# Kernel optimization log

Hardware: AMD Instinct MI355X
Metric: run time of the kernel (lower is better)

Reference implementation:

```python
import jax, jax.numpy as jnp
import numpy as np

N = 50000          # nodes
E = 1_600_000      # edges
IN = 256           # in_channels
C = 32             # hidden_channels (per-head width)
HEADS = 4
BN_EPS = 1e-5


def setup_inputs() -> dict:
    key = jax.random.key(0)
    ks = jax.random.split(key, 32)
    g = lambda k, shp, s=0.1: (jax.random.normal(k, shp, jnp.float32) * s)
    inp = {
        "x": jax.random.normal(ks[0], (N, IN), jnp.float32),
        "edge_index": jax.random.randint(ks[1], (2, E), 0, N, jnp.int64),
        "edge_attr": jax.random.uniform(ks[2], (E, 1), jnp.float32),
        # conv1 (GATConv in=IN, out=C, heads=HEADS, edge_dim=1)
        "W1": g(ks[3], (IN, HEADS * C)),
        "as1": g(ks[4], (HEADS, C)),
        "ad1": g(ks[5], (HEADS, C)),
        "We1": g(ks[6], (1, HEADS * C)),
        "ae1": g(ks[7], (HEADS, C)),
        "b1": jnp.zeros((HEADS * C,), jnp.float32),
        # bn1 (eval mode, running_mean=0, running_var=1)
        "g1": jnp.ones((HEADS * C,), jnp.float32),
        "be1": jnp.zeros((HEADS * C,), jnp.float32),
        # conv2 (GATConv in=HEADS*C, out=C, heads=1, concat=False, edge_dim=1)
        "W2": g(ks[8], (HEADS * C, C)),
        "as2": g(ks[9], (1, C)),
        "ad2": g(ks[10], (1, C)),
        "We2": g(ks[11], (1, C)),
        "ae2": g(ks[12], (1, C)),
        "b2": jnp.zeros((C,), jnp.float32),
        # bn2
        "g2": jnp.ones((C,), jnp.float32),
        "be2": jnp.zeros((C,), jnp.float32),
        # classifier: Linear(C,16) -> ReLU -> Linear(16,2)
        "Wc1": g(ks[13], (C, 16)),
        "bc1": jnp.zeros((16,), jnp.float32),
        "Wc2": g(ks[14], (16, 2)),
        "bc2": jnp.zeros((2,), jnp.float32),
        "Wr1": g(ks[15], (C, 16)),
        "br1": jnp.zeros((16,), jnp.float32),
        "Wr2": g(ks[16], (16, 1)),
        "br2": jnp.zeros((1,), jnp.float32),
    }
    return inp


def _gat_conv(x, src, dst, eattr, W, a_src, a_dst, We, a_e, bias, heads, c, concat):
    n = x.shape[0]
    xs = (x @ W).reshape(n, heads, c)                       # [N,H,C]
    al_s = (xs * a_src).sum(-1)                              # [N,H]
    al_d = (xs * a_dst).sum(-1)                              # [N,H]
    ee = (eattr @ We).reshape(-1, heads, c)                  # [E,H,C]
    al_e = (ee * a_e).sum(-1)                                # [E,H]
    alpha = al_s[src] + al_d[dst] + al_e                     # [E,H]
    alpha = jax.nn.leaky_relu(alpha, 0.2)
    # segment softmax over destination node
    mx = jax.ops.segment_max(alpha, dst, num_segments=n)
    ex = jnp.exp(alpha - mx[dst])
    den = jax.ops.segment_sum(ex, dst, num_segments=n)
    a = ex / (den[dst] + 1e-16)                              # [E,H]
    out = jax.ops.segment_sum(xs[src] * a[..., None], dst, num_segments=n)  # [N,H,C]
    out = out.reshape(n, heads * c) if concat else out.mean(axis=1)
    return out + bias


def _add_self_loops(src, dst, eattr, n):
    loop = jnp.arange(n, dtype=src.dtype)
    fill = jnp.broadcast_to(eattr.mean(axis=0, keepdims=True), (n, eattr.shape[1]))
    return (jnp.concatenate([src, loop]), jnp.concatenate([dst, loop]),
            jnp.concatenate([eattr, fill], axis=0))


def _bn_eval(x, gamma, beta):
    # running_mean=0, running_var=1 (fresh BatchNorm1d, eval mode)
    return x * (gamma / jnp.sqrt(1.0 + BN_EPS)) + beta


def reference(x, edge_index, edge_attr, W1, as1, ad1, We1, ae1, b1, g1, be1,
              W2, as2, ad2, We2, ae2, b2, g2, be2,
              Wc1, bc1, Wc2, bc2, Wr1, br1, Wr2, br2):
    n = x.shape[0]
    src, dst, ea = _add_self_loops(edge_index[0], edge_index[1], edge_attr, n)
    h = _gat_conv(x, src, dst, ea, W1, as1, ad1, We1, ae1, b1, HEADS, C, True)
    h = jax.nn.elu(_bn_eval(h, g1, be1))
    h = _gat_conv(h, src, dst, ea, W2, as2, ad2, We2, ae2, b2, 1, C, False)
    h = jax.nn.elu(_bn_eval(h, g2, be2))
    cls = jax.nn.relu(h @ Wc1 + bc1) @ Wc2 + bc2             # [N,2]
    reg = (jax.nn.relu(h @ Wr1 + br1) @ Wr2 + br2)[:, 0]     # [N]
    return cls, reg, h
```

## Files before the change

### kernel.cpp

```cpp
#include <hip/hip_runtime.h>
#include <cstdint>
#include <cstddef>

#define NN 50000
#define EE 1600000
#define IN_DIM 256
#define HC 128
#define CD 32
#define BN_RS 0.9999950000374997f

#define CAP1 96
#define CAP2 128
#define NBKT 196
#define S1_B 782
#define HIST_B 320
#define G1_B 782

typedef __attribute__((ext_vector_type(8))) short short8;
typedef __attribute__((ext_vector_type(4))) float f32x4;

__device__ __forceinline__ float lrelu(float a) { return a > 0.f ? a : 0.2f * a; }
__device__ __forceinline__ float elu(float a) { return a > 0.f ? a : (__expf(a) - 1.f); }

__device__ __forceinline__ unsigned short f2bf(float f) {
    unsigned int u = __float_as_uint(f);
    unsigned int r = (u + 0x7FFFu + ((u >> 16) & 1u)) >> 16;
    return (unsigned short)r;
}
__device__ __forceinline__ float bf2f(unsigned short b) {
    return __uint_as_float(((unsigned int)b) << 16);
}
__device__ __forceinline__ float2 bf2f2(unsigned int p) {
    float2 r;
    r.x = __uint_as_float(p << 16);
    r.y = __uint_as_float(p & 0xFFFF0000u);
    return r;
}
__device__ __forceinline__ void unpack_edge(unsigned long long p, int& s, float& eav) {
    s = (int)(unsigned int)(p & 0xFFFFFFFFull);
    eav = __uint_as_float((unsigned int)(p >> 32));
}
__device__ __forceinline__ float pick4(float a, float b, float c, float d, int h) {
    return (h & 2) ? ((h & 1) ? d : c) : ((h & 1) ? b : a);
}

__device__ __forceinline__ int block_excl_scan_256(int v, int tid, int* wsum) {
    int lane = tid & 63, wv = tid >> 6;
    int x = v;
    #pragma unroll
    for (int off = 1; off < 64; off <<= 1) {
        int y = __shfl_up(x, off);
        if (lane >= off) x += y;
    }
    if (lane == 63) wsum[wv] = x;
    __syncthreads();
    int wpre = 0;
    #pragma unroll
    for (int w = 0; w < 4; w++)
        if (w < wv) wpre += wsum[w];
    return wpre + x - v;
}

__global__ __launch_bounds__(256) void k0_prep(const float* __restrict__ W1,
                                               const float* __restrict__ W2,
                                               const float* __restrict__ We1,
                                               const float* __restrict__ ae1,
                                               const float* __restrict__ We2,
                                               const float* __restrict__ ae2,
                                               unsigned short* __restrict__ W1hi,
                                               unsigned short* __restrict__ W1lo,
                                               unsigned short* __restrict__ W2hi,
                                               unsigned short* __restrict__ W2lo,
                                               float* __restrict__ consts,
                                               int* __restrict__ bucketHist,
                                               int* __restrict__ bucketCursor,
                                               int* __restrict__ indptr) {
    int blk = blockIdx.x;
    int tid = threadIdx.x;
    if (blk < 16) {
        int t = blk * 256 + tid;
        int lane = t & 63;
        int kt = (t >> 6) & 7;
        int nt = t >> 9;
        int kbase = kt * 32 + (lane >> 4) * 8;
        int col = nt * 16 + (lane & 15);
        size_t obase = (size_t)t * 8;
        #pragma unroll
        for (int j = 0; j < 8; j++) {
            float w = W1[(size_t)(kbase + j) * HC + col];
            unsigned short h = f2bf(w);
            W1hi[obase + j] = h;
            W1lo[obase + j] = f2bf(w - bf2f(h));
        }
    } else if (blk < 18) {
        int t = (blk - 16) * 256 + tid;
        int lane = t & 63;
        int kt = (t >> 6) & 3;
        int nt = t >> 8;
        int kbase = kt * 32 + (lane >> 4) * 8;
        int col = nt * 16 + (lane & 15);
        size_t obase = (size_t)t * 8;
        #pragma unroll
        for (int j = 0; j < 8; j++) {
            float w = W2[(size_t)(kbase + j) * CD + col];
            unsigned short h = f2bf(w);
            W2hi[obase + j] = h;
            W2lo[obase + j] = f2bf(w - bf2f(h));
        }
    } else {
        if (tid < NBKT) { bucketHist[tid] = 0; bucketCursor[tid] = 0; }
        if (tid == 200) consts[0] = 0.f;
        if (tid == 201) indptr[NN] = EE;
        if (tid < 4) {
            float s = 0.f;
            for (int c = 0; c < 32; c++) s += We1[tid * 32 + c] * ae1[tid * 32 + c];
            consts[2 + tid] = s;
        } else if (tid == 4) {
            float s = 0.f;
            for (int c = 0; c < 32; c++) s += We2[c] * ae2[c];
            consts[6] = s;
        }
    }
}

__global__ __launch_bounds__(256) void kA_hist_gemm1(const int* __restrict__ ei,
                                                     const float* __restrict__ ea,
                                                     const float* __restrict__ x,
                                                     const unsigned short* __restrict__ Whi,
                                                     const unsigned short* __restrict__ Wlo,
                                                     int* __restrict__ bucketHist,
                                                     float* __restrict__ easum,
                                                     unsigned short* __restrict__ xs1b) {
    __shared__ int h[256];
    int tid = threadIdx.x;
    if (blockIdx.x < HIST_B) {
        h[tid] = 0;
        __syncthreads();
        float s = 0.f;
        for (int i = blockIdx.x * 256 + tid; i < EE; i += HIST_B * 256) {
            atomicAdd(&h[ei[EE + i] >> 8], 1);
            s += ea[i];
        }
        __syncthreads();
        if (tid < NBKT && h[tid] > 0) atomicAdd(&bucketHist[tid], h[tid]);
        #pragma unroll
        for (int off = 32; off > 0; off >>= 1) s += __shfl_xor(s, off);
        if ((tid & 63) == 0) atomicAdd(easum, s);
    } else {
        int lane = tid & 63, wv = tid >> 6;
        int row0 = (blockIdx.x - HIST_B) * 64 + wv * 16;
        if (row0 >= NN) return;
        int m = lane & 15;
        int q = lane >> 4;
        f32x4 acc[8];
        #pragma unroll
        for (int nt = 0; nt < 8; nt++) acc[nt] = {0.f, 0.f, 0.f, 0.f};
        const float* xrow = x + (size_t)(row0 + m) * IN_DIM + q * 8;
        #pragma unroll
        for (int kt = 0; kt < 8; kt++) {
            float4 v0 = *(const float4*)(xrow + kt * 32);
            float4 v1 = *(const float4*)(xrow + kt * 32 + 4);
            float vv[8] = {v0.x, v0.y, v0.z, v0.w, v1.x, v1.y, v1.z, v1.w};
            short8 ahi, alo;
            #pragma unroll
            for (int j = 0; j < 8; j++) {
                unsigned short hh = f2bf(vv[j]);
                ahi[j] = (short)hh;
                alo[j] = (short)f2bf(vv[j] - bf2f(hh));
            }
            #pragma unroll
            for (int nt = 0; nt < 8; nt++) {
                size_t fb = ((size_t)(nt * 8 + kt) * 64 + lane) * 8;
                short8 bhi = *(const short8*)(Whi + fb);
                short8 blo = *(const short8*)(Wlo + fb);
                acc[nt] = __builtin_amdgcn_mfma_f32_16x16x32_bf16(ahi, bhi, acc[nt], 0, 0, 0);
                acc[nt] = __builtin_amdgcn_mfma_f32_16x16x32_bf16(ahi, blo, acc[nt], 0, 0, 0);
                acc[nt] = __builtin_amdgcn_mfma_f32_16x16x32_bf16(alo, bhi, acc[nt], 0, 0, 0);
            }
        }
        #pragma unroll
        for (int nt = 0; nt < 8; nt++) {
            #pragma unroll
            for (int rg = 0; rg < 4; rg++) {
                int row = row0 + q * 4 + rg;
                xs1b[(size_t)row * HC + nt * 16 + m] = f2bf(acc[nt][rg]);
            }
        }
    }
}

__global__ __launch_bounds__(256) void kB_stage1_al1(const int* __restrict__ ei,
                                                     const float* __restrict__ ea,
                                                     const int* __restrict__ bucketHist,
                                                     int* __restrict__ bucketCursor,
                                                     uint2* __restrict__ Apack,
                                                     const unsigned short* __restrict__ xs1b,
                                                     const float* __restrict__ as1,
                                                     const float* __restrict__ ad1,
                                                     float* __restrict__ als,
                                                     float* __restrict__ ald) {
    __shared__ int cnt[256];
    __shared__ int basel[256];
    __shared__ int gbase[256];
    __shared__ int wsum[4];
    __shared__ int wsum2[4];
    __shared__ int sdst[2048];
    __shared__ int ssrc[2048];
    __shared__ float sea[2048];
    int tid = threadIdx.x;
    if (blockIdx.x < S1_B) {
        cnt[tid] = 0;
        int hv = (tid < NBKT) ? bucketHist[tid] : 0;
        int hexcl = block_excl_scan_256(hv, tid, wsum2);
        int base = blockIdx.x * 2048;
        int d[8], s[8], r[8], bk[8];
        float e[8];
        #pragma unroll
        for (int k = 0; k < 8; k++) {
            int i = base + k * 256 + tid;
            if (i < EE) {
                d[k] = ei[EE + i];
                s[k] = ei[i];
                e[k] = ea[i];
                bk[k] = d[k] >> 8;
                r[k] = atomicAdd(&cnt[bk[k]], 1);
            } else d[k] = -1;
        }
        __syncthreads();
        int v = cnt[tid];
        int excl = block_excl_scan_256(v, tid, wsum);
        basel[tid] = excl;
        if (tid < NBKT) gbase[tid] = hexcl + atomicAdd(&bucketCursor[tid], v);
        __syncthreads();
        #pragma unroll
        for (int k = 0; k < 8; k++) {
            if (d[k] >= 0) {
                int slot = basel[bk[k]] + r[k];
                sdst[slot] = d[k];
                ssrc[slot] = s[k];
                sea[slot] = e[k];
            }
        }
        __syncthreads();
        int total = basel[255] + cnt[255];
        for (int slot = tid; slot < total; slot += 256) {
            int dd = sdst[slot];
            int b = dd >> 8;
            int pos = gbase[b] + (slot - basel[b]);
            Apack[pos] = make_uint2((unsigned int)ssrc[slot] | ((unsigned int)(dd & 255) << 24),
                                    __float_as_uint(sea[slot]));
        }
    } else {
        int t = (blockIdx.x - S1_B) * 256 + tid;
        if (t < NN * 4) {
            int hh = t & 3;
            const unsigned int* xp = (const unsigned int*)(xs1b + (size_t)t * 32);
            const float* ap = as1 + hh * 32;
            const float* dp = ad1 + hh * 32;
            float s = 0.f, d = 0.f;
            #pragma unroll
            for (int q = 0; q < 16; q++) {
                float2 v = bf2f2(xp[q]);
                s += v.x * ap[q * 2] + v.y * ap[q * 2 + 1];
                d += v.x * dp[q * 2] + v.y * dp[q * 2 + 1];
            }
            als[t] = s;
            ald[t] = d;
        }
    }
}

__global__ __launch_bounds__(1024) void stage2_kernel(const int* __restrict__ bucketHist,
                                                      const uint2* __restrict__ Apack,
                                                      int* __restrict__ indptr,
                                                      unsigned long long* __restrict__ edgedat,
                                                      float* __restrict__ consts) {
    __shared__ int cnt[256];
    __shared__ int dbase[256];
    __shared__ int s_start;
    int tid = threadIdx.x;
    int b = blockIdx.x;
    if (b == 0 && tid == 0) consts[1] = consts[0] / (float)EE;
    if (tid < 64) {
        int p = 0;
        for (int i = tid; i < b; i += 64) p += bucketHist[i];
        #pragma unroll
        for (int off = 32; off > 0; off >>= 1) p += __shfl_xor(p, off);
        if (tid == 0) s_start = p;
    }
    if (tid < 256) cnt[tid] = 0;
    __syncthreads();
    int start = s_start;
    int end = start + bucketHist[b];
    for (int i = start + tid; i < end; i += 1024) atomicAdd(&cnt[Apack[i].x >> 24], 1);
    __syncthreads();
    if (tid < 64) {
        int b4 = tid * 4;
        int c0 = cnt[b4], c1 = cnt[b4 + 1], c2 = cnt[b4 + 2], c3 = cnt[b4 + 3];
        int t = c0 + c1 + c2 + c3;
        int x = t;
        #pragma unroll
        for (int off = 1; off < 64; off <<= 1) {
            int y = __shfl_up(x, off);
            if (tid >= off) x += y;
        }
        int e0 = x - t;
        dbase[b4] = e0;
        dbase[b4 + 1] = e0 + c0;
        dbase[b4 + 2] = e0 + c0 + c1;
        dbase[b4 + 3] = e0 + c0 + c1 + c2;
    }
    __syncthreads();
    if (tid < 256) {
        int n = b * 256 + tid;
        if (n < NN) indptr[n] = start + dbase[tid];
        cnt[tid] = 0;
    }
    __syncthreads();
    for (int i = start + tid; i < end; i += 1024) {
        uint2 p = Apack[i];
        int dl = p.x >> 24;
        int r = atomicAdd(&cnt[dl], 1);
        int pos = start + dbase[dl] + r;
        edgedat[pos] = (unsigned long long)(p.x & 0xFFFFFFu) |
                       ((unsigned long long)p.y << 32);
    }
}

#define ACC4(vv, ww) { float2 p0_ = bf2f2((vv).x); float2 p1_ = bf2f2((vv).y); \
    acc0 += p0_.x * (ww); acc1 += p0_.y * (ww); acc2 += p1_.x * (ww); acc3 += p1_.y * (ww); }

#define H1P 136
__global__ __launch_bounds__(256, 8) void gat1_gemm2(
    const unsigned short* __restrict__ xs1b, const float* __restrict__ als,
    const float* __restrict__ ald, const unsigned long long* __restrict__ edgedat,
    const int* __restrict__ indptr, const float* __restrict__ consts,
    const float* __restrict__ b1, const float* __restrict__ g1,
    const float* __restrict__ be1,
    const unsigned short* __restrict__ W2hi, const unsigned short* __restrict__ W2lo,
    const float* __restrict__ as2, const float* __restrict__ ad2,
    unsigned short* __restrict__ xs2b, float* __restrict__ als2,
    float* __restrict__ ald2) {
    __shared__ __align__(16) float exbuf[8][CAP1][4];
    __shared__ int srcbuf[8][CAP1];
    __shared__ __align__(16) unsigned short h1hi_s[8][H1P];
    __shared__ __align__(16) unsigned short h1lo_s[8][H1P];
    int tid = threadIdx.x;
    int l = tid & 31;
    int nb = tid >> 5;
    int n = blockIdx.x * 8 + nb;
    int start = indptr[n];
    int deg = indptr[n + 1] - start;
    float ea_mean = consts[1];
    float ce0 = consts[2], ce1 = consts[3], ce2 = consts[4], ce3 = consts[5];
    float4 a4d = *(const float4*)(ald + (size_t)n * 4);
    float4 a4s = *(const float4*)(als + (size_t)n * 4);
    float ex00 = __expf(lrelu(a4s.x + a4d.x + ea_mean * ce0));
    float ex01 = __expf(lrelu(a4s.y + a4d.y + ea_mean * ce1));
    float ex02 = __expf(lrelu(a4s.z + a4d.z + ea_mean * ce2));
    float ex03 = __expf(lrelu(a4s.w + a4d.w + ea_mean * ce3));
    float sm0 = 0.f, sm1 = 0.f, sm2 = 0.f, sm3 = 0.f;
    const unsigned long long* edp = edgedat + start;
    for (int i = l; i < deg; i += 32) {
        int s; float eav;
        unpack_edge(edp[i], s, eav);
        float4 v4 = *(const float4*)(als + (size_t)s * 4);
        float4 ex4;
        ex4.x = __expf(lrelu(v4.x + a4d.x + eav * ce0)); sm0 += ex4.x;
        ex4.y = __expf(lrelu(v4.y + a4d.y + eav * ce1)); sm1 += ex4.y;
        ex4.z = __expf(lrelu(v4.z + a4d.z + eav * ce2)); sm2 += ex4.z;
        ex4.w = __expf(lrelu(v4.w + a4d.w + eav * ce3)); sm3 += ex4.w;
        if (i < CAP1) {
            srcbuf[nb][i] = s * (HC * 2);
            *(float4*)(&exbuf[nb][i][0]) = ex4;
        }
    }
    #pragma unroll
    for (int off = 16; off > 0; off >>= 1) {
        sm0 += __shfl_xor(sm0, off);
        sm1 += __shfl_xor(sm1, off);
        sm2 += __shfl_xor(sm2, off);
        sm3 += __shfl_xor(sm3, off);
    }
    int h2 = l >> 3;
    float ex0sel = pick4(ex00, ex01, ex02, ex03, h2);
    float inv = 1.0f / (pick4(sm0, sm1, sm2, sm3, h2) + ex0sel + 1e-16f);
    int mcap = deg < CAP1 ? deg : CAP1;
    const char* xb = (const char*)xs1b + (size_t)l * 8;
    float acc0, acc1, acc2, acc3;
    {
        uint2 v = *(const uint2*)(xb + (size_t)n * (HC * 2));
        float2 p0 = bf2f2(v.x), p1 = bf2f2(v.y);
        acc0 = p0.x * ex0sel; acc1 = p0.y * ex0sel;
        acc2 = p1.x * ex0sel; acc3 = p1.y * ex0sel;
    }
    int i = 0;
    for (; i + 8 <= mcap; i += 8) {
        int o0 = srcbuf[nb][i + 0], o1 = srcbuf[nb][i + 1];
        int o2 = srcbuf[nb][i + 2], o3 = srcbuf[nb][i + 3];
        int o4 = srcbuf[nb][i + 4], o5 = srcbuf[nb][i + 5];
        int o6 = srcbuf[nb][i + 6], o7 = srcbuf[nb][i + 7];
        float w0 = exbuf[nb][i + 0][h2], w1 = exbuf[nb][i + 1][h2];
        float w2 = exbuf[nb][i + 2][h2], w3 = exbuf[nb][i + 3][h2];
        float w4 = exbuf[nb][i + 4][h2], w5 = exbuf[nb][i + 5][h2];
        float w6 = exbuf[nb][i + 6][h2], w7 = exbuf[nb][i + 7][h2];
        uint2 v0 = *(const uint2*)(xb + o0);
        uint2 v1 = *(const uint2*)(xb + o1);
        uint2 v2 = *(const uint2*)(xb + o2);
        uint2 v3 = *(const uint2*)(xb + o3);
        uint2 v4 = *(const uint2*)(xb + o4);
        uint2 v5 = *(const uint2*)(xb + o5);
        uint2 v6 = *(const uint2*)(xb + o6);
        uint2 v7 = *(const uint2*)(xb + o7);
        ACC4(v0, w0); ACC4(v1, w1); ACC4(v2, w2); ACC4(v3, w3);
        ACC4(v4, w4); ACC4(v5, w5); ACC4(v6, w6); ACC4(v7, w7);
    }
    for (; i < mcap; i++) {
        int o = srcbuf[nb][i];
        float w = exbuf[nb][i][h2];
        uint2 v = *(const uint2*)(xb + o);
        ACC4(v, w);
    }
    if (deg > CAP1) {
        float aldsel = pick4(a4d.x, a4d.y, a4d.z, a4d.w, h2);
        float cesel = pick4(ce0, ce1, ce2, ce3, h2);
        for (int j = CAP1; j < deg; j++) {
            int s; float eav;
            unpack_edge(edp[j], s, eav);
            float w = __expf(lrelu(als[(size_t)s * 4 + h2] + aldsel + eav * cesel));
            uint2 v = *(const uint2*)(xb + (size_t)s * (HC * 2));
            ACC4(v, w);
        }
    }
    acc0 *= inv; acc1 *= inv; acc2 *= inv; acc3 *= inv;
    int c = l * 4;
    float4 bb = *(const float4*)(b1 + c);
    float4 gg = *(const float4*)(g1 + c);
    float4 eb = *(const float4*)(be1 + c);
    float o0 = elu((acc0 + bb.x) * (gg.x * BN_RS) + eb.x);
    float o1 = elu((acc1 + bb.y) * (gg.y * BN_RS) + eb.y);
    float o2 = elu((acc2 + bb.z) * (gg.z * BN_RS) + eb.z);
    float o3 = elu((acc3 + bb.w) * (gg.w * BN_RS) + eb.w);
    unsigned short h0 = f2bf(o0), h1v = f2bf(o1), h2v = f2bf(o2), h3v = f2bf(o3);
    unsigned short l0 = f2bf(o0 - bf2f(h0)), l1 = f2bf(o1 - bf2f(h1v));
    unsigned short l2 = f2bf(o2 - bf2f(h2v)), l3 = f2bf(o3 - bf2f(h3v));
    uint2 hiw, low;
    hiw.x = (unsigned int)h0 | ((unsigned int)h1v << 16);
    hiw.y = (unsigned int)h2v | ((unsigned int)h3v << 16);
    low.x = (unsigned int)l0 | ((unsigned int)l1 << 16);
    low.y = (unsigned int)l2 | ((unsigned int)l3 << 16);
    *(uint2*)(&h1hi_s[nb][c]) = hiw;
    *(uint2*)(&h1lo_s[nb][c]) = low;
    __syncthreads();
    if (tid >= 64) return;

    int lane = tid;
    int m = lane & 15, q = lane >> 4;
    int r8 = m & 7;
    f32x4 g2acc0 = {0.f, 0.f, 0.f, 0.f};
    f32x4 g2acc1 = {0.f, 0.f, 0.f, 0.f};
    #pragma unroll
    for (int kt = 0; kt < 4; kt++) {
        short8 ahi = *(const short8*)(&h1hi_s[r8][q * 8 + kt * 32]);
        short8 alo = *(const short8*)(&h1lo_s[r8][q * 8 + kt * 32]);
        size_t fb0 = ((size_t)kt * 64 + lane) * 8;
        size_t fb1 = ((size_t)(4 + kt) * 64 + lane) * 8;
        short8 bhi0 = *(const short8*)(W2hi + fb0);
        short8 blo0 = *(const short8*)(W2lo + fb0);
        short8 bhi1 = *(const short8*)(W2hi + fb1);
        short8 blo1 = *(const short8*)(W2lo + fb1);
        g2acc0 = __builtin_amdgcn_mfma_f32_16x16x32_bf16(ahi, bhi0, g2acc0, 0, 0, 0);
        g2acc0 = __builtin_amdgcn_mfma_f32_16x16x32_bf16(ahi, blo0, g2acc0, 0, 0, 0);
        g2acc0 = __builtin_amdgcn_mfma_f32_16x16x32_bf16(alo, bhi0, g2acc0, 0, 0, 0);
        g2acc1 = __builtin_amdgcn_mfma_f32_16x16x32_bf16(ahi, bhi1, g2acc1, 0, 0, 0);
        g2acc1 = __builtin_amdgcn_mfma_f32_16x16x32_bf16(ahi, blo1, g2acc1, 0, 0, 0);
        g2acc1 = __builtin_amdgcn_mfma_f32_16x16x32_bf16(alo, bhi1, g2acc1, 0, 0, 0);
    }
    int n0 = blockIdx.x * 8;
    float a0 = as2[m], a1 = as2[m + 16];
    float d0 = ad2[m], d1 = ad2[m + 16];
    #pragma unroll
    for (int rg = 0; rg < 4; rg++) {
        int rloc = q * 4 + rg;
        float s = g2acc0[rg] * a0 + g2acc1[rg] * a1;
        float d = g2acc0[rg] * d0 + g2acc1[rg] * d1;
        #pragma unroll
        for (int off = 1; off < 16; off <<= 1) {
            s += __shfl_xor(s, off);
            d += __shfl_xor(d, off);
        }
        if (rloc < 8) {
            int row = n0 + rloc;
            xs2b[(size_t)row * CD + m]      = f2bf(g2acc0[rg]);
            xs2b[(size_t)row * CD + 16 + m] = f2bf(g2acc1[rg]);
            if (m == 0) { als2[row] = s; ald2[row] = d; }
        }
    }
}

__global__ __launch_bounds__(256) void gat2_agg(
    const unsigned short* __restrict__ xs2b, const float* __restrict__ als,
    const float* __restrict__ ald, const unsigned long long* __restrict__ edgedat,
    const int* __restrict__ indptr, const float* __restrict__ consts,
    const float* __restrict__ b2, const float* __restrict__ g2, const float* __restrict__ be2,
    const float* __restrict__ Wc1, const float* __restrict__ bc1,
    const float* __restrict__ Wc2, const float* __restrict__ bc2,
    const float* __restrict__ Wr1, const float* __restrict__ br1,
    const float* __restrict__ Wr2, const float* __restrict__ br2,
    float* __restrict__ hout, float* __restrict__ cls, float* __restrict__ reg) {
    __shared__ float exbuf[4][CAP2];
    __shared__ int srcbuf[4][CAP2];
    __shared__ __align__(16) float hbuf[4][32];
    int wv = threadIdx.x >> 6;
    int lane = threadIdx.x & 63;
    int n = blockIdx.x * 4 + wv;
    int start = indptr[n];
    int deg = indptr[n + 1] - start;
    float ea_mean = consts[1];
    float ce = consts[6];
    float aldn = ald[n];
    float ex0 = __expf(lrelu(als[n] + aldn + ea_mean * ce));
    float sm = 0.f;
    const unsigned long long* edp = edgedat + start;
    for (int i = lane; i < deg; i += 64) {
        int s; float eav;
        unpack_edge(edp[i], s, eav);
        float exv = __expf(lrelu(als[s] + aldn + eav * ce));
        if (i < CAP2) { srcbuf[wv][i] = s * (CD * 2); exbuf[wv][i] = exv; }
        sm += exv;
    }
    #pragma unroll
    for (int off = 32; off > 0; off >>= 1) sm += __shfl_xor(sm, off);
    float invd = 1.0f / (sm + ex0 + 1e-16f);
    int mcap = deg < CAP2 ? deg : CAP2;
    int oct = lane >> 3, lo = lane & 7;
    const char* xb = (const char*)xs2b + (size_t)lo * 8;
    float acc0 = 0.f, acc1 = 0.f, acc2 = 0.f, acc3 = 0.f;
    if (oct == 0) {
        uint2 v = *(const uint2*)(xb + (size_t)n * (CD * 2));
        float2 p0 = bf2f2(v.x), p1 = bf2f2(v.y);
        acc0 = p0.x * ex0; acc1 = p0.y * ex0; acc2 = p1.x * ex0; acc3 = p1.y * ex0;
    }
    for (int i = oct; i < mcap; i += 8) {
        float w = exbuf[wv][i];
        int o = srcbuf[wv][i];
        uint2 v = *(const uint2*)(xb + o);
        ACC4(v, w);
    }
    for (int i = CAP2 + oct; i < deg; i += 8) {
        int s; float eav;
        unpack_edge(edp[i], s, eav);
        float w = __expf(lrelu(als[s] + aldn + eav * ce));
        uint2 v = *(const uint2*)(xb + (size_t)s * (CD * 2));
        ACC4(v, w);
    }
    #pragma unroll
    for (int off = 8; off < 64; off <<= 1) {
        acc0 += __shfl_xor(acc0, off);
        acc1 += __shfl_xor(acc1, off);
        acc2 += __shfl_xor(acc2, off);
        acc3 += __shfl_xor(acc3, off);
    }
    if (lane < 8) {
        int c = lo * 4;
        float4 bb = *(const float4*)(b2 + c);
        float4 gg = *(const float4*)(g2 + c);
        float4 eb = *(const float4*)(be2 + c);
        float o0 = elu((acc0 * invd + bb.x) * (gg.x * BN_RS) + eb.x);
        float o1 = elu((acc1 * invd + bb.y) * (gg.y * BN_RS) + eb.y);
        float o2 = elu((acc2 * invd + bb.z) * (gg.z * BN_RS) + eb.z);
        float o3 = elu((acc3 * invd + bb.w) * (gg.w * BN_RS) + eb.w);
        *(float4*)(&hbuf[wv][c]) = make_float4(o0, o1, o2, o3);
        *(float4*)(hout + (size_t)n * CD + c) = make_float4(o0, o1, o2, o3);
    }
    float r0 = 0.f, r1 = 0.f;
    if (lane < 32) {
        int j = lane & 15;
        bool iscls = lane < 16;
        float s = iscls ? bc1[j] : br1[j];
        #pragma unroll
        for (int cc = 0; cc < 32; cc++) {
            float w = iscls ? Wc1[cc * 16 + j] : Wr1[cc * 16 + j];
            s += hbuf[wv][cc] * w;
        }
        s = fmaxf(s, 0.f);
        if (iscls) { r0 = s * Wc2[j * 2]; r1 = s * Wc2[j * 2 + 1]; }
        else       { r0 = s * Wr2[j]; }
    }
    #pragma unroll
    for (int off = 1; off < 16; off <<= 1) {
        r0 += __shfl_xor(r0, off);
        r1 += __shfl_xor(r1, off);
    }
    if (lane == 0)  *(float2*)(cls + (size_t)n * 2) = make_float2(r0 + bc2[0], r1 + bc2[1]);
    if (lane == 16) reg[n] = r0 + br2[0];
}

extern "C" void kernel_launch(void* const* d_in, const int* in_sizes, int n_in,
                              void* d_out, int out_size, void* d_ws, size_t ws_size,
                              hipStream_t stream) {
    const float* x   = (const float*)d_in[0];
    const int*   ei  = (const int*)d_in[1];
    const float* ea  = (const float*)d_in[2];
    const float* W1  = (const float*)d_in[3];
    const float* as1 = (const float*)d_in[4];
    const float* ad1 = (const float*)d_in[5];
    const float* We1 = (const float*)d_in[6];
    const float* ae1 = (const float*)d_in[7];
    const float* b1  = (const float*)d_in[8];
    const float* g1  = (const float*)d_in[9];
    const float* be1 = (const float*)d_in[10];
    const float* W2  = (const float*)d_in[11];
    const float* as2 = (const float*)d_in[12];
    const float* ad2 = (const float*)d_in[13];
    const float* We2 = (const float*)d_in[14];
    const float* ae2 = (const float*)d_in[15];
    const float* b2  = (const float*)d_in[16];
    const float* g2  = (const float*)d_in[17];
    const float* be2 = (const float*)d_in[18];
    const float* Wc1 = (const float*)d_in[19];
    const float* bc1 = (const float*)d_in[20];
    const float* Wc2 = (const float*)d_in[21];
    const float* bc2 = (const float*)d_in[22];
    const float* Wr1 = (const float*)d_in[23];
    const float* br1 = (const float*)d_in[24];
    const float* Wr2 = (const float*)d_in[25];
    const float* br2 = (const float*)d_in[26];

    char* ws = (char*)d_ws;
    unsigned short* xs1b = (unsigned short*)(ws + 0);
    uint2* Apack         = (uint2*)(ws + 12800000);
    unsigned short* xs2b = (unsigned short*)(ws + 38400000);
    float* als1          = (float*)(ws + 41600000);
    float* ald1          = (float*)(ws + 42400000);
    float* als2          = (float*)(ws + 43200000);
    float* ald2          = (float*)(ws + 43400000);
    float* consts        = (float*)(ws + 43600000);
    int*   bucketHist    = (int*)(ws + 43600128);
    int*   bucketCursor  = (int*)(ws + 43601920);
    int*   indptr        = (int*)(ws + 43602816);
    unsigned long long* edgedat = (unsigned long long*)(ws + 43802824);
    unsigned short* W1hi = (unsigned short*)(ws + 56602832);
    unsigned short* W1lo = (unsigned short*)(ws + 56668368);
    unsigned short* W2hi = (unsigned short*)(ws + 56733904);
    unsigned short* W2lo = (unsigned short*)(ws + 56742096);

    float* out_cls = (float*)d_out;
    float* out_reg = out_cls + 2 * NN;
    float* out_h   = out_cls + 3 * NN;

    k0_prep<<<19, 256, 0, stream>>>(W1, W2, We1, ae1, We2, ae2,
                                    W1hi, W1lo, W2hi, W2lo, consts,
                                    bucketHist, bucketCursor, indptr);
    kA_hist_gemm1<<<HIST_B + G1_B, 256, 0, stream>>>(ei, ea, x, W1hi, W1lo,
                                                     bucketHist, consts, xs1b);
    kB_stage1_al1<<<S1_B + 782, 256, 0, stream>>>(ei, ea, bucketHist, bucketCursor,
                                                  Apack, xs1b, as1, ad1, als1, ald1);
    stage2_kernel<<<NBKT, 1024, 0, stream>>>(bucketHist, Apack, indptr, edgedat, consts);

    gat1_gemm2<<<NN / 8, 256, 0, stream>>>(xs1b, als1, ald1, edgedat, indptr, consts,
                                           b1, g1, be1, W2hi, W2lo, as2, ad2,
                                           xs2b, als2, ald2);
    gat2_agg<<<NN / 4, 256, 0, stream>>>(xs2b, als2, ald2, edgedat, indptr, consts,
                                         b2, g2, be2, Wc1, bc1, Wc2, bc2,
                                         Wr1, br1, Wr2, br2, out_h, out_cls, out_reg);
}
```

Before: 325.0 us.

## Use half-wave per node in GAT2 aggregation and prefetch x rows in GEMM1

```diff
diff --git a/kernel.cpp b/kernel.cpp
--- a/kernel.cpp
+++ b/kernel.cpp
@@ -152,14 +152,20 @@
         if (row0 >= NN) return;
         int m = lane & 15;
         int q = lane >> 4;
+        const float* xrow = x + (size_t)(row0 + m) * IN_DIM + q * 8;
+        float4 xv[16];
+        #pragma unroll
+        for (int kt = 0; kt < 8; kt++) {
+            xv[kt * 2]     = *(const float4*)(xrow + kt * 32);
+            xv[kt * 2 + 1] = *(const float4*)(xrow + kt * 32 + 4);
+        }
         f32x4 acc[8];
         #pragma unroll
         for (int nt = 0; nt < 8; nt++) acc[nt] = {0.f, 0.f, 0.f, 0.f};
-        const float* xrow = x + (size_t)(row0 + m) * IN_DIM + q * 8;
         #pragma unroll
         for (int kt = 0; kt < 8; kt++) {
-            float4 v0 = *(const float4*)(xrow + kt * 32);
-            float4 v1 = *(const float4*)(xrow + kt * 32 + 4);
+            float4 v0 = xv[kt * 2];
+            float4 v1 = xv[kt * 2 + 1];
             float vv[8] = {v0.x, v0.y, v0.z, v0.w, v1.x, v1.y, v1.z, v1.w};
             short8 ahi, alo;
             #pragma unroll
@@ -508,12 +514,13 @@
     const float* __restrict__ Wr1, const float* __restrict__ br1,
     const float* __restrict__ Wr2, const float* __restrict__ br2,
     float* __restrict__ hout, float* __restrict__ cls, float* __restrict__ reg) {
-    __shared__ float exbuf[4][CAP2];
-    __shared__ int srcbuf[4][CAP2];
-    __shared__ __align__(16) float hbuf[4][32];
-    int wv = threadIdx.x >> 6;
-    int lane = threadIdx.x & 63;
-    int n = blockIdx.x * 4 + wv;
+    __shared__ float exbuf[8][CAP2];
+    __shared__ int srcbuf[8][CAP2];
+    __shared__ __align__(16) float hbuf[8][32];
+    int tid = threadIdx.x;
+    int l = tid & 31;
+    int nb = tid >> 5;
+    int n = blockIdx.x * 8 + nb;
     int start = indptr[n];
     int deg = indptr[n + 1] - start;
     float ea_mean = consts[1];
@@ -522,18 +529,18 @@
     float ex0 = __expf(lrelu(als[n] + aldn + ea_mean * ce));
     float sm = 0.f;
     const unsigned long long* edp = edgedat + start;
-    for (int i = lane; i < deg; i += 64) {
+    for (int i = l; i < deg; i += 32) {
         int s; float eav;
         unpack_edge(edp[i], s, eav);
         float exv = __expf(lrelu(als[s] + aldn + eav * ce));
-        if (i < CAP2) { srcbuf[wv][i] = s * (CD * 2); exbuf[wv][i] = exv; }
+        if (i < CAP2) { srcbuf[nb][i] = s * (CD * 2); exbuf[nb][i] = exv; }
         sm += exv;
     }
     #pragma unroll
-    for (int off = 32; off > 0; off >>= 1) sm += __shfl_xor(sm, off);
+    for (int off = 16; off > 0; off >>= 1) sm += __shfl_xor(sm, off);
     float invd = 1.0f / (sm + ex0 + 1e-16f);
     int mcap = deg < CAP2 ? deg : CAP2;
-    int oct = lane >> 3, lo = lane & 7;
+    int oct = l >> 3, lo = l & 7;
     const char* xb = (const char*)xs2b + (size_t)lo * 8;
     float acc0 = 0.f, acc1 = 0.f, acc2 = 0.f, acc3 = 0.f;
     if (oct == 0) {
@@ -541,13 +548,13 @@
         float2 p0 = bf2f2(v.x), p1 = bf2f2(v.y);
         acc0 = p0.x * ex0; acc1 = p0.y * ex0; acc2 = p1.x * ex0; acc3 = p1.y * ex0;
     }
-    for (int i = oct; i < mcap; i += 8) {
-        float w = exbuf[wv][i];
-        int o = srcbuf[wv][i];
+    for (int i = oct; i < mcap; i += 4) {
+        float w = exbuf[nb][i];
+        int o = srcbuf[nb][i];
         uint2 v = *(const uint2*)(xb + o);
         ACC4(v, w);
     }
-    for (int i = CAP2 + oct; i < deg; i += 8) {
+    for (int i = CAP2 + oct; i < deg; i += 4) {
         int s; float eav;
         unpack_edge(edp[i], s, eav);
         float w = __expf(lrelu(als[s] + aldn + eav * ce));
@@ -555,13 +562,13 @@
         ACC4(v, w);
     }
     #pragma unroll
-    for (int off = 8; off < 64; off <<= 1) {
+    for (int off = 8; off < 32; off <<= 1) {
         acc0 += __shfl_xor(acc0, off);
         acc1 += __shfl_xor(acc1, off);
         acc2 += __shfl_xor(acc2, off);
         acc3 += __shfl_xor(acc3, off);
     }
-    if (lane < 8) {
+    if (l < 8) {
         int c = lo * 4;
         float4 bb = *(const float4*)(b2 + c);
         float4 gg = *(const float4*)(g2 + c);
@@ -570,18 +577,18 @@
         float o1 = elu((acc1 * invd + bb.y) * (gg.y * BN_RS) + eb.y);
         float o2 = elu((acc2 * invd + bb.z) * (gg.z * BN_RS) + eb.z);
         float o3 = elu((acc3 * invd + bb.w) * (gg.w * BN_RS) + eb.w);
-        *(float4*)(&hbuf[wv][c]) = make_float4(o0, o1, o2, o3);
+        *(float4*)(&hbuf[nb][c]) = make_float4(o0, o1, o2, o3);
         *(float4*)(hout + (size_t)n * CD + c) = make_float4(o0, o1, o2, o3);
     }
     float r0 = 0.f, r1 = 0.f;
-    if (lane < 32) {
-        int j = lane & 15;
-        bool iscls = lane < 16;
+    {
+        int j = l & 15;
+        bool iscls = l < 16;
         float s = iscls ? bc1[j] : br1[j];
         #pragma unroll
         for (int cc = 0; cc < 32; cc++) {
             float w = iscls ? Wc1[cc * 16 + j] : Wr1[cc * 16 + j];
-            s += hbuf[wv][cc] * w;
+            s += hbuf[nb][cc] * w;
         }
         s = fmaxf(s, 0.f);
         if (iscls) { r0 = s * Wc2[j * 2]; r1 = s * Wc2[j * 2 + 1]; }
@@ -592,8 +599,8 @@
         r0 += __shfl_xor(r0, off);
         r1 += __shfl_xor(r1, off);
     }
-    if (lane == 0)  *(float2*)(cls + (size_t)n * 2) = make_float2(r0 + bc2[0], r1 + bc2[1]);
-    if (lane == 16) reg[n] = r0 + br2[0];
+    if (l == 0)  *(float2*)(cls + (size_t)n * 2) = make_float2(r0 + bc2[0], r1 + bc2[1]);
+    if (l == 16) reg[n] = r0 + br2[0];
 }
 
 extern "C" void kernel_launch(void* const* d_in, const int* in_sizes, int n_in,
@@ -661,7 +668,7 @@
     gat1_gemm2<<<NN / 8, 256, 0, stream>>>(xs1b, als1, ald1, edgedat, indptr, consts,
                                            b1, g1, be1, W2hi, W2lo, as2, ad2,
                                            xs2b, als2, ald2);
-    gat2_agg<<<NN / 4, 256, 0, stream>>>(xs2b, als2, ald2, edgedat, indptr, consts,
+    gat2_agg<<<NN / 8, 256, 0, stream>>>(xs2b, als2, ald2, edgedat, indptr, consts,
                                          b2, g2, be2, Wc1, bc1, Wc2, bc2,
                                          Wr1, br1, Wr2, br2, out_h, out_cls, out_reg);
 }
```

Result: faster. 316.9 us, median of 2 (-2.5%).
